# Performance work log

Hardware: AMD Instinct MI355X
Metric: run time of the kernel (lower is better)

Reference implementation:

```python
import jax, jax.numpy as jnp
import numpy as np

CLAMP = 15  # relative positions clipped to [-15, 15], shifted to [0, 30]


def setup_inputs() -> dict:
    key = jax.random.key(0)
    ks = jax.random.split(key, 8)
    B, L, C, P = 2, 512, 256, 128
    return {
        "single_repr": jax.random.normal(ks[0], (B, L, C), jnp.float32),
        "pair_bias": jax.random.normal(ks[1], (B, L, L, 2), jnp.float32),
        "mask": jax.random.uniform(ks[2], (B, L), jnp.float32),
        "w_outer": jax.random.normal(ks[3], (C * C, P), jnp.float32) * (1.0 / C),
        "b_outer": jax.random.normal(ks[4], (P,), jnp.float32) * 0.02,
        "pos_embed": jax.random.normal(ks[5], (32, P), jnp.float32) * 0.02,
        "w_bias": jax.random.normal(ks[6], (2, P), jnp.float32) * 0.02,
        "b_bias": jax.random.normal(ks[7], (P,), jnp.float32) * 0.02,
    }


def reference(single_repr, pair_bias, mask, w_outer, b_outer, pos_embed, w_bias, b_bias):
    B, L, C = single_repr.shape
    P = w_outer.shape[-1]
    # Fused outer-product + projection: z[b,i,j,p] = sum_{c,d} s[b,i,c] s[b,j,d] W[c,d,p]
    # done as two matmuls, never materializing the [B,L,L,C,C] tensor.
    W = w_outer.reshape(C, C, P)
    tmp = jnp.einsum('bjd,cdp->bjcp', single_repr, W)          # [B,L,C,P]
    z = jnp.einsum('bic,bjcp->bijp', single_repr, tmp) + b_outer  # [B,L,L,P]
    # pair bias projection (pair_bias_dim=2 != pair_dim -> project)
    z = z + (pair_bias @ w_bias + b_bias)
    # relative-position embedding
    pos = jnp.arange(L)
    rel_pos = jnp.clip(pos[:, None] - pos[None, :], -CLAMP, CLAMP) + CLAMP  # [L,L] in [0,30]
    z = z + pos_embed[rel_pos]
    # pair mask
    pair_mask = mask[:, :, None] * mask[:, None, :]
    z = z * pair_mask[..., None]
    return z
```

## Files before the change

kernel.cpp:

```cpp
#include <hip/hip_runtime.h>
#include <stdint.h>

#define GLOBAL_AS __attribute__((address_space(1)))
#define LDS_AS    __attribute__((address_space(3)))

typedef __attribute__((ext_vector_type(8))) short short8;
typedef __attribute__((ext_vector_type(4))) float f32x4;
typedef __attribute__((ext_vector_type(4))) float float4v;
typedef __attribute__((ext_vector_type(2))) float float2v;
typedef __attribute__((ext_vector_type(4))) unsigned short ushort4v;

static constexpr int Bc = 2;
static constexpr int Lc = 512;
static constexpr int Cc = 256;
static constexpr int Pc = 128;
static constexpr int NP = Pc * Cc;
static constexpr size_t TMPB = (size_t)Lc * NP;

__device__ __forceinline__ unsigned short f2bf(float x) {
  unsigned int u = __builtin_bit_cast(unsigned int, x);
  u += 0x7FFFu + ((u >> 16) & 1u);
  return (unsigned short)(u >> 16);
}

__device__ __forceinline__ void gload_lds16(const void* g, void* l) {
  __builtin_amdgcn_global_load_lds((const GLOBAL_AS unsigned int*)g,
                                   (LDS_AS unsigned int*)l, 16, 0, 0);
}

__global__ void convert_s_kernel(const float* __restrict__ s,
                                 unsigned short* __restrict__ out) {
  const int idx = (blockIdx.x * 256 + threadIdx.x) * 4;
  float4v v = *(const float4v*)&s[idx];
  ushort4v o;
  #pragma unroll
  for (int i = 0; i < 4; ++i) o[i] = f2bf(v[i]);
  *(ushort4v*)&out[idx] = o;
}

__global__ void prep_w_kernel(const float* __restrict__ w,
                              unsigned short* __restrict__ wA) {
  __shared__ unsigned short lds[128 * 258];
  const int c = blockIdx.x;
  const int t = threadIdx.x;
  const float* wc = w + (size_t)c * (Cc * Pc);
  #pragma unroll 4
  for (int it = 0; it < 128; ++it) {
    const int idx = it * 256 + t;
    const int d = idx >> 7, p = idx & 127;
    lds[p * 258 + d] = f2bf(wc[idx]);
  }
  __syncthreads();
  #pragma unroll 4
  for (int it = 0; it < 128; ++it) {
    const int idx = it * 256 + t;
    const int p = idx >> 8, d = idx & 255;
    wA[(size_t)p * 65536 + (size_t)c * 256 + d] = lds[p * 258 + d];
  }
}

__device__ __forceinline__ void run_gemm_k256(
    const unsigned short* __restrict__ gA,
    const unsigned short* __restrict__ gB,
    unsigned short (&As)[2][256 * 64],
    unsigned short (&Bs)[2][256 * 64],
    const int tid, const int wave, const int wr, const int wc,
    const int lr, const int lk,
    f32x4 (&acc)[8][4]) {
  auto stage = [&](int sel, int t) {
    const int k0 = t * 64;
    #pragma unroll
    for (int r = 0; r < 4; ++r) {
      const int idx = r * 512 + tid;
      const int row = idx >> 3, col = (idx & 7) << 3;
      gload_lds16(&gA[(size_t)row * 256 + k0 + col],
                  &As[sel][(size_t)(r * 512 + wave * 64) * 8]);
    }
    #pragma unroll
    for (int r = 0; r < 4; ++r) {
      const int idx = r * 512 + tid;
      const int row = idx >> 3, col = (idx & 7) << 3;
      gload_lds16(&gB[(size_t)row * 256 + k0 + col],
                  &Bs[sel][(size_t)(r * 512 + wave * 64) * 8]);
    }
  };

  stage(0, 0);
  __syncthreads();
  #pragma unroll
  for (int t = 0; t < 4; ++t) {
    const int cur = t & 1;
    if (t < 3) stage(cur ^ 1, t + 1);
    #pragma unroll
    for (int kk = 0; kk < 2; ++kk) {
      short8 a[8], b[4];
      #pragma unroll
      for (int m = 0; m < 8; ++m)
        a[m] = *(const short8*)&As[cur][(wr * 128 + m * 16 + lr) * 64 + kk * 32 + lk];
      #pragma unroll
      for (int n = 0; n < 4; ++n)
        b[n] = *(const short8*)&Bs[cur][(wc * 64 + n * 16 + lr) * 64 + kk * 32 + lk];
      #pragma unroll
      for (int m = 0; m < 8; ++m)
        #pragma unroll
        for (int n = 0; n < 4; ++n)
          acc[m][n] = __builtin_amdgcn_mfma_f32_16x16x32_bf16(a[m], b[n], acc[m][n], 0, 0, 0);
    }
    __syncthreads();
  }
}

__global__ __launch_bounds__(512, 2) void gemm1_k(
    const unsigned short* __restrict__ sbf,
    const unsigned short* __restrict__ wA,
    unsigned short* __restrict__ tmpT) {
  __shared__ unsigned short As[2][256 * 64];
  __shared__ unsigned short Bs[2][256 * 64];
  const int tid = threadIdx.x;
  const int wave = tid >> 6, lane = tid & 63;
  const int wr = wave >> 2, wc = wave & 3;
  const int lr = lane & 15, lk = (lane >> 4) << 3;
  const int p = blockIdx.x;
  const int j0 = blockIdx.y * 256;
  const int z = blockIdx.z;

  const unsigned short* gA = wA + (size_t)p * 65536;
  const unsigned short* gB = sbf + (size_t)z * Lc * Cc + (size_t)j0 * 256;

  f32x4 acc[8][4];
  const f32x4 zero = {0.f, 0.f, 0.f, 0.f};
  #pragma unroll
  for (int m = 0; m < 8; ++m)
    #pragma unroll
    for (int n = 0; n < 4; ++n) acc[m][n] = zero;

  run_gemm_k256(gA, gB, As, Bs, tid, wave, wr, wc, lr, lk, acc);

  unsigned short* tT = tmpT + (size_t)z * TMPB;
  const int cq = wr * 128 + ((lane >> 4) << 2);
  #pragma unroll
  for (int n = 0; n < 4; ++n) {
    const int j = j0 + wc * 64 + n * 16 + lr;
    unsigned short* dst = tT + (size_t)j * NP + p * 256 + cq;
    #pragma unroll
    for (int m = 0; m < 8; ++m) {
      ushort4v o;
      #pragma unroll
      for (int q = 0; q < 4; ++q) o[q] = f2bf(acc[m][n][q]);
      *(ushort4v*)&dst[m * 16] = o;
    }
  }
}

__global__ __launch_bounds__(512, 2) void gemm2_k(
    const unsigned short* __restrict__ sbf,
    const unsigned short* __restrict__ tmpT,
    const float* __restrict__ pair_bias,
    const float* __restrict__ mask,
    const float* __restrict__ b_outer,
    const float* __restrict__ pos_embed,
    const float* __restrict__ w_bias,
    const float* __restrict__ b_bias,
    float* __restrict__ out) {
  __shared__ unsigned short As[2][256 * 64];
  __shared__ unsigned short Bs[2][256 * 64];
  const int tid = threadIdx.x;
  const int wave = tid >> 6, lane = tid & 63;
  const int wr = wave >> 2, wc = wave & 3;
  const int lr = lane & 15, lk = (lane >> 4) << 3;
  const int jt = blockIdx.x;
  const int i0 = blockIdx.y * 256;
  const int z = blockIdx.z;

  const unsigned short* gA = tmpT + (size_t)z * TMPB + (size_t)jt * 65536;
  const unsigned short* gB = sbf + (size_t)z * Lc * Cc + (size_t)i0 * 256;

  f32x4 acc[8][4];
  const f32x4 zero = {0.f, 0.f, 0.f, 0.f};
  #pragma unroll
  for (int m = 0; m < 8; ++m)
    #pragma unroll
    for (int n = 0; n < 4; ++n) acc[m][n] = zero;

  run_gemm_k256(gA, gB, As, Bs, tid, wave, wr, wc, lr, lk, acc);

  const int j = jt * 2 + wr;
  const int pq = (lane >> 4) << 2;
  const float mj = mask[z * Lc + j];

  float4v base8[8];
  #pragma unroll
  for (int m = 0; m < 8; ++m) {
    const int pp = m * 16 + pq;
    base8[m] = *(const float4v*)&b_outer[pp] + *(const float4v*)&b_bias[pp];
  }

  #pragma unroll
  for (int n = 0; n < 4; ++n) {
    const int i = i0 + wc * 64 + n * 16 + lr;
    const float sc = mask[z * Lc + i] * mj;
    const size_t rowoff = ((size_t)(z * Lc + i)) * Lc + j;
    const float2v pb = *(const float2v*)&pair_bias[rowoff * 2];
    int rel = i - j;
    rel = rel < -15 ? -15 : (rel > 15 ? 15 : rel);
    rel += 15;
    const float* pe_row = pos_embed + rel * Pc;
    float* drow = out + rowoff * Pc;
    #pragma unroll
    for (int m = 0; m < 8; ++m) {
      const int pp = m * 16 + pq;
      const float4v wb0 = *(const float4v*)&w_bias[pp];
      const float4v wb1 = *(const float4v*)&w_bias[Pc + pp];
      const float4v pe4 = *(const float4v*)&pe_row[pp];
      float4v v = acc[m][n] + base8[m] + pb[0] * wb0 + pb[1] * wb1 + pe4;
      *(float4v*)&drow[pp] = v * sc;
    }
  }
}

extern "C" void kernel_launch(void* const* d_in, const int* in_sizes, int n_in,
                              void* d_out, int out_size, void* d_ws, size_t ws_size,
                              hipStream_t stream) {
  const float* s         = (const float*)d_in[0];
  const float* pair_bias = (const float*)d_in[1];
  const float* mask      = (const float*)d_in[2];
  const float* w_outer   = (const float*)d_in[3];
  const float* b_outer   = (const float*)d_in[4];
  const float* pos_embed = (const float*)d_in[5];
  const float* w_bias    = (const float*)d_in[6];
  const float* b_bias    = (const float*)d_in[7];
  float* out = (float*)d_out;

  unsigned char* ws = (unsigned char*)d_ws;
  unsigned short* s_bf = (unsigned short*)ws;
  unsigned short* wA   = (unsigned short*)(ws + (512u << 10));
  unsigned short* tmpT = (unsigned short*)(ws + (512u << 10) + (16u << 20));

  convert_s_kernel<<<256, 256, 0, stream>>>(s, s_bf);
  prep_w_kernel<<<256, 256, 0, stream>>>(w_outer, wA);
  gemm1_k<<<dim3(128, 2, 2), 512, 0, stream>>>(s_bf, wA, tmpT);
  gemm2_k<<<dim3(256, 2, 2), 512, 0, stream>>>(s_bf, tmpT, pair_bias, mask,
                                               b_outer, pos_embed, w_bias,
                                               b_bias, out);
}
```

Baseline: 427.6 us.

## Merge prep kernels and remap GEMM grids to 1D with XCD-aware block swizzle

Fuses the s-conversion and weight-transpose kernels into one launch, removing a kernel launch. Both GEMMs move to a 1D grid whose block index is permuted so that consecutive blocks scheduled on the same XCD (bid&7) share operand tiles (same p or same jt), which is meant to improve L2 reuse across the chiplets. The batch dimension is folded into the j index. Behaviour should be identical, but the indexing is more intricate and depends on an assumed round-robin dispatch of blocks across XCDs.

Result: no change. 435.1 us (+1.8%).

```diff
diff --git a/kernel.cpp b/kernel.cpp
--- a/kernel.cpp
+++ b/kernel.cpp
@@ -28,21 +28,22 @@
                                    (LDS_AS unsigned int*)l, 16, 0, 0);
 }
 
-__global__ void convert_s_kernel(const float* __restrict__ s,
-                                 unsigned short* __restrict__ out) {
-  const int idx = (blockIdx.x * 256 + threadIdx.x) * 4;
-  float4v v = *(const float4v*)&s[idx];
-  ushort4v o;
-  #pragma unroll
-  for (int i = 0; i < 4; ++i) o[i] = f2bf(v[i]);
-  *(ushort4v*)&out[idx] = o;
-}
-
-__global__ void prep_w_kernel(const float* __restrict__ w,
-                              unsigned short* __restrict__ wA) {
+__global__ void prep_kernel(const float* __restrict__ w,
+                            unsigned short* __restrict__ wA,
+                            const float* __restrict__ s,
+                            unsigned short* __restrict__ s_bf) {
+  const int t = threadIdx.x;
+  if (blockIdx.x >= 256) {
+    const int idx = ((blockIdx.x - 256) * 256 + t) * 4;
+    float4v v = *(const float4v*)&s[idx];
+    ushort4v o;
+    #pragma unroll
+    for (int i = 0; i < 4; ++i) o[i] = f2bf(v[i]);
+    *(ushort4v*)&s_bf[idx] = o;
+    return;
+  }
   __shared__ unsigned short lds[128 * 258];
   const int c = blockIdx.x;
-  const int t = threadIdx.x;
   const float* wc = w + (size_t)c * (Cc * Pc);
   #pragma unroll 4
   for (int it = 0; it < 128; ++it) {
@@ -120,12 +121,13 @@
   const int wave = tid >> 6, lane = tid & 63;
   const int wr = wave >> 2, wc = wave & 3;
   const int lr = lane & 15, lk = (lane >> 4) << 3;
-  const int p = blockIdx.x;
-  const int j0 = blockIdx.y * 256;
-  const int z = blockIdx.z;
+
+  const int bid = blockIdx.x;
+  const int f = (bid & 7) * 64 + (bid >> 3);
+  const int p = f >> 2, nt = f & 3;
 
   const unsigned short* gA = wA + (size_t)p * 65536;
-  const unsigned short* gB = sbf + (size_t)z * Lc * Cc + (size_t)j0 * 256;
+  const unsigned short* gB = sbf + (size_t)nt * 65536;
 
   f32x4 acc[8][4];
   const f32x4 zero = {0.f, 0.f, 0.f, 0.f};
@@ -136,12 +138,11 @@
 
   run_gemm_k256(gA, gB, As, Bs, tid, wave, wr, wc, lr, lk, acc);
 
-  unsigned short* tT = tmpT + (size_t)z * TMPB;
   const int cq = wr * 128 + ((lane >> 4) << 2);
   #pragma unroll
   for (int n = 0; n < 4; ++n) {
-    const int j = j0 + wc * 64 + n * 16 + lr;
-    unsigned short* dst = tT + (size_t)j * NP + p * 256 + cq;
+    const int zj = nt * 256 + wc * 64 + n * 16 + lr;
+    unsigned short* dst = tmpT + (size_t)zj * NP + p * 256 + cq;
     #pragma unroll
     for (int m = 0; m < 8; ++m) {
       ushort4v o;
@@ -168,12 +169,14 @@
   const int wave = tid >> 6, lane = tid & 63;
   const int wr = wave >> 2, wc = wave & 3;
   const int lr = lane & 15, lk = (lane >> 4) << 3;
-  const int jt = blockIdx.x;
-  const int i0 = blockIdx.y * 256;
-  const int z = blockIdx.z;
-
-  const unsigned short* gA = tmpT + (size_t)z * TMPB + (size_t)jt * 65536;
-  const unsigned short* gB = sbf + (size_t)z * Lc * Cc + (size_t)i0 * 256;
+
+  const int bid = blockIdx.x;
+  const int f = (bid & 7) * 128 + (bid >> 3);
+  const int jt = f >> 1, i0t = f & 1;
+  const int z = jt >> 8;
+
+  const unsigned short* gA = tmpT + (size_t)jt * 65536;
+  const unsigned short* gB = sbf + (size_t)(z * Lc + i0t * 256) * Cc;
 
   f32x4 acc[8][4];
   const f32x4 zero = {0.f, 0.f, 0.f, 0.f};
@@ -184,7 +187,8 @@
 
   run_gemm_k256(gA, gB, As, Bs, tid, wave, wr, wc, lr, lk, acc);
 
-  const int j = jt * 2 + wr;
+  const int zj = jt * 2 + wr;
+  const int j = zj & (Lc - 1);
   const int pq = (lane >> 4) << 2;
   const float mj = mask[z * Lc + j];
 
@@ -197,7 +201,7 @@
 
   #pragma unroll
   for (int n = 0; n < 4; ++n) {
-    const int i = i0 + wc * 64 + n * 16 + lr;
+    const int i = i0t * 256 + wc * 64 + n * 16 + lr;
     const float sc = mask[z * Lc + i] * mj;
     const size_t rowoff = ((size_t)(z * Lc + i)) * Lc + j;
     const float2v pb = *(const float2v*)&pair_bias[rowoff * 2];
@@ -236,10 +240,8 @@
   unsigned short* wA   = (unsigned short*)(ws + (512u << 10));
   unsigned short* tmpT = (unsigned short*)(ws + (512u << 10) + (16u << 20));
 
-  convert_s_kernel<<<256, 256, 0, stream>>>(s, s_bf);
-  prep_w_kernel<<<256, 256, 0, stream>>>(w_outer, wA);
-  gemm1_k<<<dim3(128, 2, 2), 512, 0, stream>>>(s_bf, wA, tmpT);
-  gemm2_k<<<dim3(256, 2, 2), 512, 0, stream>>>(s_bf, tmpT, pair_bias, mask,
-                                               b_outer, pos_embed, w_bias,
-                                               b_bias, out);
-}
+  prep_kernel<<<512, 256, 0, stream>>>(w_outer, wA, s, s_bf);
+  gemm1_k<<<512, 512, 0, stream>>>(s_bf, wA, tmpT);
+  gemm2_k<<<1024, 512, 0, stream>>>(s_bf, tmpT, pair_bias, mask,
+                                    b_outer, pos_embed, w_bias, b_bias, out);
+}
```
